# Performance work log

Hardware: AMD Instinct MI355X
Metric: run time of the kernel (lower is better)

## Reference

```python
import jax, jax.numpy as jnp
import numpy as np

N = 50000      # num_labels (nodes)
HID = 64       # hidden_dim
HEADS = 4
CH = 16        # hidden_dim // 4 per head
R = 4          # relations
E = 200000     # edges per relation
DEPTH = 2
SLOPE = 0.2    # GATv2 leaky_relu negative slope
EPS = 1e-5     # LayerNorm eps


def layer_norm(x, g, b):
    mu = jnp.mean(x, axis=-1, keepdims=True)
    var = jnp.mean((x - mu) ** 2, axis=-1, keepdims=True)
    return (x - mu) / jnp.sqrt(var + EPS) * g + b


def setup_inputs() -> dict:
    key = jax.random.key(0)
    ks = jax.random.split(key, 8)
    # edges with src != dst (PyG remove_self_loops is then a no-op)
    src = jax.random.randint(ks[0], (R, E), 0, N, dtype=jnp.int32)
    off = jax.random.randint(ks[1], (R, E), 1, N, dtype=jnp.int32)
    dst = ((src + off) % N).astype(jnp.int32)
    edge_index = jnp.stack([src, dst], axis=1)  # [R, 2, E]
    s = 1.0 / np.sqrt(HID)
    return {
        "label_embeddings": jax.random.normal(ks[2], (N, HID), jnp.float32) * 0.5,
        "entry_w": jax.random.normal(ks[3], (HID, HID), jnp.float32) * s,
        "entry_b": jnp.zeros((HID,), jnp.float32),
        "entry_ln_g": jnp.ones((HID,), jnp.float32),
        "entry_ln_b": jnp.zeros((HID,), jnp.float32),
        "conv_wl": jax.random.normal(ks[4], (DEPTH, R, HID, HEADS * CH), jnp.float32) * s,
        "conv_wr": jax.random.normal(ks[5], (DEPTH, R, HID, HEADS * CH), jnp.float32) * s,
        "conv_att": jax.random.normal(ks[6], (DEPTH, R, HEADS, CH), jnp.float32) * (1.0 / np.sqrt(CH)),
        "conv_bias": jnp.zeros((DEPTH, R, HEADS * CH), jnp.float32),
        "norm_g": jnp.ones((HID,), jnp.float32),
        "norm_b": jnp.zeros((HID,), jnp.float32),
        "edge_index": edge_index,
    }


def _gatv2_layer(x, wl, wr, att, bias, src, dst):
    """One GATv2Conv over one relation. x:[N,HID]; returns [N, HEADS*CH]."""
    xl = (x @ wl).reshape(N, HEADS, CH)  # source transform
    xr = (x @ wr).reshape(N, HEADS, CH)  # target transform
    m = xl[src] + xr[dst]                          # [E+N, HEADS, CH]
    e = jnp.einsum('ehc,hc->eh', jax.nn.leaky_relu(m, SLOPE), att)  # [E+N, HEADS]
    # segment softmax over incoming edges of each dst node
    emax = jax.ops.segment_max(e, dst, num_segments=N)  # [N, HEADS]
    a = jnp.exp(e - emax[dst])
    denom = jax.ops.segment_sum(a, dst, num_segments=N)
    alpha = a / denom[dst]                          # every node has a self-loop -> denom > 0
    msg = xl[src] * alpha[..., None]                # [E+N, HEADS, CH]
    out = jax.ops.segment_sum(msg, dst, num_segments=N).reshape(N, HEADS * CH)
    return out + bias


def reference(label_embeddings, entry_w, entry_b, entry_ln_g, entry_ln_b,
              conv_wl, conv_wr, conv_att, conv_bias, norm_g, norm_b, edge_index):
    x = jax.nn.gelu(layer_norm(label_embeddings @ entry_w + entry_b, entry_ln_g, entry_ln_b),
                    approximate=False)
    loop = jnp.arange(N, dtype=edge_index.dtype)
    for layer in range(DEPTH):
        outs = []
        for r in range(R):
            src = jnp.concatenate([edge_index[r, 0], loop])  # add self-loops (PyG default)
            dst = jnp.concatenate([edge_index[r, 1], loop])
            outs.append(_gatv2_layer(x, conv_wl[layer, r], conv_wr[layer, r],
                                     conv_att[layer, r], conv_bias[layer, r], src, dst))
        x = sum(outs) / R                              # HeteroConv aggr='mean'
        x = layer_norm(jax.nn.gelu(x, approximate=False), norm_g, norm_b)  # dropout = identity (eval)
    return x
```

## Files before the change

kernel.cpp:

```cpp
#include <hip/hip_runtime.h>
#include <hip/hip_bf16.h>

#define NN 50000
#define RR 4
#define EE 200000
#define CAP 32

typedef __hip_bfloat16 bf16;
typedef __attribute__((ext_vector_type(8))) short short8;
typedef __attribute__((ext_vector_type(4))) float float4v;
typedef __attribute__((ext_vector_type(2))) float float2v;

__device__ __forceinline__ float b2f(bf16 v) { return __bfloat162float(v); }
__device__ __forceinline__ unsigned short f2bu(float v) {
    bf16 h = __float2bfloat16(v);
    return *(unsigned short*)&h;
}
__device__ __forceinline__ float ldf(const void* p, int i, int isbf) {
    return isbf ? __bfloat162float(((const bf16*)p)[i]) : ((const float*)p)[i];
}
__device__ __forceinline__ int dtype_isbf(const void* lg) {
    return ((const unsigned*)lg)[0] == 0x3F803F80u;
}
__device__ __forceinline__ float gelu_exact(float x) {
    return 0.5f * x * (1.0f + erff(x * 0.70710678118654752f));
}
__device__ __forceinline__ float2v bp2(unsigned u) {
    float2v f;
    f.x = __uint_as_float(u << 16);
    f.y = __uint_as_float(u & 0xffff0000u);
    return f;
}
__device__ __forceinline__ float2v lrelu2(float2v m) {
    float2v s = m * 0.2f;
    float2v r;
    r.x = fmaxf(m.x, s.x);
    r.y = fmaxf(m.y, s.y);
    return r;
}

#define PW_ENTRY_W 0
#define PW_ENTRY_B 4096
#define PW_LN_G    4160
#define PW_LN_B    4224
#define PW_WL      4288
#define PW_ATT     69824
#define PW_BIAS    70336
#define PW_NG      70848
#define PW_NB      70912
#define PW_TOT     70976

#define WT_ELEMS (2 * RR * 128 * 64)

__global__ __launch_bounds__(1024) void cvt_k(const void* ew, const void* eb, const void* lg,
                                              const void* lb, const void* wl, const void* wr,
                                              const void* at, const void* bi, const void* ng,
                                              const void* nb,
                                              float* __restrict__ P, bf16* __restrict__ WT,
                                              int* __restrict__ cnt) {
    int i = blockIdx.x * 1024 + threadIdx.x;
    int isbf = dtype_isbf(lg);
    if (i < RR * NN) cnt[i] = 0;
    if (i < WT_ELEMS) {
        int k = i & 63;
        int c = (i >> 6) & 127;
        int lr = i >> 13;
        float v = (c < 64) ? ldf(wl, (lr * 64 + k) * 64 + c, isbf)
                           : ldf(wr, (lr * 64 + k) * 64 + (c - 64), isbf);
        WT[i] = __float2bfloat16(v);
    }
    if (i < PW_TOT) {
        const void* src = nullptr;
        int off = 0;
        if (i < PW_ENTRY_B)      { src = ew; off = i - PW_ENTRY_W; }
        else if (i < PW_LN_G)    { src = eb; off = i - PW_ENTRY_B; }
        else if (i < PW_LN_B)    { src = lg; off = i - PW_LN_G; }
        else if (i < PW_WL)      { src = lb; off = i - PW_LN_B; }
        else if (i < PW_ATT)     { src = nullptr; }
        else if (i < PW_BIAS)    { src = at; off = i - PW_ATT; }
        else if (i < PW_NG)      { src = bi; off = i - PW_BIAS; }
        else if (i < PW_NB)      { src = ng; off = i - PW_NG; }
        else                     { src = nb; off = i - PW_NB; }
        if (src) P[i] = ldf(src, off, isbf);
    }
}

#define SCAT_BLOCKS 782
#define ENTRY_BLOCKS 2500
#define ENTRY_WAVES (ENTRY_BLOCKS * 4)
__global__ __launch_bounds__(256) void scent_k(const int* __restrict__ ei,
                                               int* __restrict__ cnt,
                                               unsigned short* __restrict__ col,
                                               const void* __restrict__ emb,
                                               const void* __restrict__ lg,
                                               const float* __restrict__ P,
                                               bf16* __restrict__ xout) {
    int b = blockIdx.x;
    if (b < SCAT_BLOCKS) {
        int base = b * 1024 + threadIdx.x;
#pragma unroll
        for (int j = 0; j < 4; j++) {
            int idx = base + j * 256;
            if (idx < RR * EE) {
                int r = idx / EE;
                int e = idx - r * EE;
                int s = ei[r * 2 * EE + e];
                int d = ei[r * 2 * EE + EE + e];
                int p = atomicAdd(&cnt[r * NN + d], 1);
                if (p < CAP) col[((size_t)r * NN + d) * CAP + p] = (unsigned short)s;
            }
        }
        return;
    }
    int wv = (b - SCAT_BLOCKS) * 4 + (threadIdx.x >> 6);
    int c = threadIdx.x & 63;
    int isbf = dtype_isbf(lg);
    for (int j = 0; j < 5; j++) {
        int node = wv + j * ENTRY_WAVES;
        float ev = ldf(emb, node * 64 + c, isbf);
        float acc = 0.f;
#pragma unroll 8
        for (int k = 0; k < 64; k++) {
            float xv = __shfl(ev, k, 64);
            acc += xv * P[PW_ENTRY_W + k * 64 + c];
        }
        acc += P[PW_ENTRY_B + c];
        float s = acc;
#pragma unroll
        for (int m = 1; m < 64; m <<= 1) s += __shfl_xor(s, m, 64);
        float mu = s * (1.f / 64.f);
        float d = acc - mu;
        float vs = d * d;
#pragma unroll
        for (int m = 1; m < 64; m <<= 1) vs += __shfl_xor(vs, m, 64);
        float var = vs * (1.f / 64.f);
        float y = d * rsqrtf(var + 1e-5f) * P[PW_LN_G + c] + P[PW_LN_B + c];
        xout[node * 64 + c] = __float2bfloat16(gelu_exact(y));
    }
}

#define GR 80
__global__ __launch_bounds__(256) void gemm_m(const bf16* __restrict__ X,
                                              const bf16* __restrict__ WTlayer,
                                              bf16* __restrict__ xlB,
                                              bf16* __restrict__ xrB) {
    int r = blockIdx.y;
    const short* Xs = (const short*)X;
    const short* WT = (const short*)(WTlayer + (size_t)r * 8192);
    bf16* xl = xlB + (size_t)r * NN * 64;
    bf16* xr = xrB + (size_t)r * NN * 64;

    __shared__ float sh[16 * 132];
    int t = threadIdx.x;
    int w = t >> 6;
    int lane = t & 63;
    int m = lane & 15, kq = lane >> 4;
    int row0 = blockIdx.x * GR;

    short8 b0[2], b1[2];
    int c0t[2];
#pragma unroll
    for (int tile = 0; tile < 2; tile++) {
        int ct = w * 2 + tile;
        int c0 = ct * 16 + m;
        c0t[tile] = c0;
        const short* bp = WT + c0 * 64 + kq * 8;
        b0[tile] = *(const short8*)bp;
        b1[tile] = *(const short8*)(bp + 32);
    }

    const short* ap = Xs + (row0 + m) * 64 + kq * 8;
    short8 a0 = *(const short8*)ap;
    short8 a1 = *(const short8*)(ap + 32);

    for (int g = 0; g < 5; g++) {
        short8 na0, na1;
        if (g < 4) {
            const short* np = ap + (g + 1) * 16 * 64;
            na0 = *(const short8*)np;
            na1 = *(const short8*)(np + 32);
        }
#pragma unroll
        for (int tile = 0; tile < 2; tile++) {
            float4v acc = {0.f, 0.f, 0.f, 0.f};
            asm volatile(
                "v_mfma_f32_16x16x32_bf16 %0, %1, %2, %0\n\t"
                "v_mfma_f32_16x16x32_bf16 %0, %3, %4, %0\n\t"
                "s_nop 7\n\t"
                "s_nop 7"
                : "+v"(acc)
                : "v"(a0), "v"(b0[tile]), "v"(a1), "v"(b1[tile]));
#pragma unroll
            for (int i = 0; i < 4; i++) sh[(kq * 4 + i) * 132 + c0t[tile]] = acc[i];
        }
        __syncthreads();
        {
            int row = t >> 4, cg = (t & 15) * 8;
            float v0 = sh[row * 132 + cg + 0], v1 = sh[row * 132 + cg + 1];
            float v2 = sh[row * 132 + cg + 2], v3 = sh[row * 132 + cg + 3];
            float v4 = sh[row * 132 + cg + 4], v5 = sh[row * 132 + cg + 5];
            float v6 = sh[row * 132 + cg + 6], v7 = sh[row * 132 + cg + 7];
            uint4 u;
            u.x = ((unsigned)f2bu(v1) << 16) | f2bu(v0);
            u.y = ((unsigned)f2bu(v3) << 16) | f2bu(v2);
            u.z = ((unsigned)f2bu(v5) << 16) | f2bu(v4);
            u.w = ((unsigned)f2bu(v7) << 16) | f2bu(v6);
            size_t grow = row0 + g * 16 + row;
            if (cg < 64) *(uint4*)&xl[grow * 64 + cg] = u;
            else         *(uint4*)&xr[grow * 64 + (cg - 64)] = u;
        }
        __syncthreads();
        a0 = na0; a1 = na1;
    }
}

__device__ __forceinline__ void edge_accum(uint4 u0, uint4 u1, bool act,
                                           const float2v at2[8], const float2v xr2[8],
                                           float2v A2[8], float& D) {
    float2v x2[8];
    x2[0] = bp2(u0.x); x2[1] = bp2(u0.y); x2[2] = bp2(u0.z); x2[3] = bp2(u0.w);
    x2[4] = bp2(u1.x); x2[5] = bp2(u1.y); x2[6] = bp2(u1.z); x2[7] = bp2(u1.w);
    float2v t2 = (float2v){0.f, 0.f};
#pragma unroll
    for (int i = 0; i < 8; i++)
        t2 = t2 + lrelu2(x2[i] + xr2[i]) * at2[i];
    float tt = t2.x + t2.y;
    float p = act ? exp2f(tt) : 0.f;
    D += p;
    float2v p2 = (float2v){p, p};
#pragma unroll
    for (int i = 0; i < 8; i++) A2[i] = A2[i] + p2 * x2[i];
}

__global__ __launch_bounds__(256) void aggfin_k(const bf16* __restrict__ xlB,
                                                const bf16* __restrict__ xrB,
                                                const float* __restrict__ attL,
                                                const float* __restrict__ biasL,
                                                const int* __restrict__ cnt,
                                                const unsigned short* __restrict__ col,
                                                const float* __restrict__ P,
                                                const void* __restrict__ lg,
                                                void* __restrict__ outp,
                                                int finalOut) {
    __shared__ float shRes[RR][4][68];
    int t = threadIdx.x;
    int r = t >> 6;
    int lane = t & 63;
    int nodeBase = blockIdx.x * 4;
    int nn = lane >> 4, es = (lane >> 2) & 3, h = lane & 3;
    int node = nodeBase + nn;

    const unsigned* xl = (const unsigned*)(xlB + (size_t)r * NN * 64);
    const unsigned* xr = (const unsigned*)(xrB + (size_t)r * NN * 64);
    const float* att = attL + r * 64;
    const float* bias = biasL + r * 64;
    const unsigned short* bucket = col + ((size_t)r * NN + node) * CAP;

    int cn_raw = cnt[r * NN + node];
    int c0raw = (es > 0) ? (int)bucket[es - 1] : node;
    int c1raw = (int)bucket[es + 3];
    const uint4* qr = (const uint4*)(xr + (size_t)node * 32 + h * 8);
    uint4 r0 = qr[0], r1 = qr[1];

    unsigned s0 = (unsigned)c0raw < (unsigned)NN ? (unsigned)c0raw : (unsigned)(NN - 1);
    unsigned s1 = (unsigned)c1raw < (unsigned)NN ? (unsigned)c1raw : (unsigned)(NN - 1);
    const uint4* q0 = (const uint4*)(xl + (size_t)s0 * 32 + h * 8);
    uint4 u0 = q0[0], u1 = q0[1];
    const uint4* q1 = (const uint4*)(xl + (size_t)s1 * 32 + h * 8);
    uint4 w0 = q1[0], w1 = q1[1];

    float2v at2[8], xr2[8];
    {
        const float4* apv = (const float4*)(att + h * 16);
#pragma unroll
        for (int i = 0; i < 4; i++) {
            float4 a = apv[i];
            at2[2 * i].x = a.x * 1.44269504f; at2[2 * i].y = a.y * 1.44269504f;
            at2[2 * i + 1].x = a.z * 1.44269504f; at2[2 * i + 1].y = a.w * 1.44269504f;
        }
        xr2[0] = bp2(r0.x); xr2[1] = bp2(r0.y); xr2[2] = bp2(r0.z); xr2[3] = bp2(r0.w);
        xr2[4] = bp2(r1.x); xr2[5] = bp2(r1.y); xr2[6] = bp2(r1.z); xr2[7] = bp2(r1.w);
    }
    int cn = cn_raw > CAP ? CAP : cn_raw;
    int total = cn + 1;
    int kmax = total;
    kmax = max(kmax, __shfl_xor(kmax, 16, 64));
    kmax = max(kmax, __shfl_xor(kmax, 32, 64));

    float2v A2[8];
#pragma unroll
    for (int i = 0; i < 8; i++) A2[i] = (float2v){0.f, 0.f};
    float D = 0.f;

    edge_accum(u0, u1, es < total, at2, xr2, A2, D);
    edge_accum(w0, w1, es + 4 < total, at2, xr2, A2, D);

    for (int k = es + 8; k < kmax; k += 4) {
        bool act = k < total;
        int sr = act ? (int)bucket[k - 1] : node;
        const uint4* q = (const uint4*)(xl + (size_t)sr * 32 + h * 8);
        uint4 t0 = q[0], t1 = q[1];
        edge_accum(t0, t1, act, at2, xr2, A2, D);
    }

    D += __shfl_xor(D, 4, 64);
    D += __shfl_xor(D, 8, 64);
#pragma unroll
    for (int i = 0; i < 8; i++) {
        A2[i].x += __shfl_xor(A2[i].x, 4, 64);
        A2[i].x += __shfl_xor(A2[i].x, 8, 64);
        A2[i].y += __shfl_xor(A2[i].y, 4, 64);
        A2[i].y += __shfl_xor(A2[i].y, 8, 64);
    }
    if (es == 0) {
        float inv = __builtin_amdgcn_rcpf(D);
        const float4* bp = (const float4*)(bias + h * 16);
        float* dst = &shRes[r][nn][h * 16];
#pragma unroll
        for (int i = 0; i < 4; i++) {
            float4 b = bp[i];
            dst[4 * i + 0] = A2[2 * i].x * inv + b.x;
            dst[4 * i + 1] = A2[2 * i].y * inv + b.y;
            dst[4 * i + 2] = A2[2 * i + 1].x * inv + b.z;
            dst[4 * i + 3] = A2[2 * i + 1].y * inv + b.w;
        }
    }
    __syncthreads();
    int wn = t >> 6, c = t & 63;
    float v = shRes[0][wn][c] + shRes[1][wn][c] + shRes[2][wn][c] + shRes[3][wn][c];
    v = gelu_exact(v * 0.25f);
    float s = v;
#pragma unroll
    for (int m = 1; m < 64; m <<= 1) s += __shfl_xor(s, m, 64);
    float mu = s * (1.f / 64.f);
    float d = v - mu;
    float vs = d * d;
#pragma unroll
    for (int m = 1; m < 64; m <<= 1) vs += __shfl_xor(vs, m, 64);
    float var = vs * (1.f / 64.f);
    float y = d * rsqrtf(var + 1e-5f) * P[PW_NG + c] + P[PW_NB + c];
    size_t o = (size_t)(nodeBase + wn) * 64 + c;
    if (!finalOut) {
        ((bf16*)outp)[o] = __float2bfloat16(y);
    } else {
        if (dtype_isbf(lg)) ((bf16*)outp)[o] = __float2bfloat16(y);
        else                ((float*)outp)[o] = y;
    }
}

extern "C" void kernel_launch(void* const* d_in, const int* in_sizes, int n_in,
                              void* d_out, int out_size, void* d_ws, size_t ws_size,
                              hipStream_t stream) {
    const void* emb = d_in[0];
    const void* lg  = d_in[3];
    const int*  ei  = (const int*)d_in[11];

    const size_t BUF = (size_t)NN * 64;

    bf16* X   = (bf16*)d_ws;
    bf16* XL  = X + BUF;
    bf16* XR  = XL + RR * BUF;
    bf16* WT  = XR + RR * BUF;
    float* P  = (float*)(WT + WT_ELEMS);
    int* cnt  = (int*)(P + PW_TOT);
    unsigned short* col = (unsigned short*)(cnt + RR * NN);

    int cvtN = RR * NN;
    cvt_k<<<(cvtN + 1023) / 1024, 1024, 0, stream>>>(d_in[1], d_in[2], d_in[3], d_in[4],
                                                     d_in[5], d_in[6], d_in[7], d_in[8],
                                                     d_in[9], d_in[10], P, WT, cnt);

    scent_k<<<SCAT_BLOCKS + ENTRY_BLOCKS, 256, 0, stream>>>(ei, cnt, col, emb, lg, P, X);

    int gemmBlocks = NN / GR;
    int nodeBlocks = NN / 4;

    for (int l = 0; l < 2; l++) {
        gemm_m<<<dim3(gemmBlocks, RR), 256, 0, stream>>>(X, WT + (size_t)l * RR * 8192, XL, XR);
        aggfin_k<<<nodeBlocks, 256, 0, stream>>>(
            XL, XR, P + PW_ATT + (size_t)l * RR * 64, P + PW_BIAS + (size_t)l * RR * 64,
            cnt, col, P, lg, (l == 0) ? (void*)X : d_out, l);
    }
}
```

Before: 334.8 us.

## Replace fixed-capacity adjacency buckets with CSR built via histogram, scan, scatter

Replaces the per-node CAP=32 bucket array with a compact CSR layout. A histogram pass records each edge's slot, a three-kernel prefix scan produces row pointers, and the scatter runs inside the first-layer GEMM launch as extra blocks. This shrinks the adjacency footprint and removes the capacity truncation, which improves gather locality in the aggregation kernel. The cost is three extra small launches and an extra read of the edge list.

Result: faster. 323.6 us (-3.3%).

```diff
diff --git a/kernel.cpp b/kernel.cpp
--- a/kernel.cpp
+++ b/kernel.cpp
@@ -4,14 +4,12 @@
 #define NN 50000
 #define RR 4
 #define EE 200000
-#define CAP 32
 
 typedef __hip_bfloat16 bf16;
 typedef __attribute__((ext_vector_type(8))) short short8;
 typedef __attribute__((ext_vector_type(4))) float float4v;
 typedef __attribute__((ext_vector_type(2))) float float2v;
 
-__device__ __forceinline__ float b2f(bf16 v) { return __bfloat162float(v); }
 __device__ __forceinline__ unsigned short f2bu(float v) {
     bf16 h = __float2bfloat16(v);
     return *(unsigned short*)&h;
@@ -51,6 +49,9 @@
 #define PW_TOT     70976
 
 #define WT_ELEMS (2 * RR * 128 * 64)
+#define SCAN_N (RR * NN)
+#define NSB 196
+#define ESB 196
 
 __global__ __launch_bounds__(1024) void cvt_k(const void* ew, const void* eb, const void* lg,
                                               const void* lb, const void* wl, const void* wr,
@@ -60,7 +61,7 @@
                                               int* __restrict__ cnt) {
     int i = blockIdx.x * 1024 + threadIdx.x;
     int isbf = dtype_isbf(lg);
-    if (i < RR * NN) cnt[i] = 0;
+    if (i < SCAN_N) cnt[i] = 0;
     if (i < WT_ELEMS) {
         int k = i & 63;
         int c = (i >> 6) & 127;
@@ -85,18 +86,18 @@
     }
 }
 
-#define SCAT_BLOCKS 782
+#define HIST_BLOCKS 782
 #define ENTRY_BLOCKS 2500
 #define ENTRY_WAVES (ENTRY_BLOCKS * 4)
 __global__ __launch_bounds__(256) void scent_k(const int* __restrict__ ei,
                                                int* __restrict__ cnt,
-                                               unsigned short* __restrict__ col,
+                                               unsigned char* __restrict__ slot8,
                                                const void* __restrict__ emb,
                                                const void* __restrict__ lg,
                                                const float* __restrict__ P,
                                                bf16* __restrict__ xout) {
     int b = blockIdx.x;
-    if (b < SCAT_BLOCKS) {
+    if (b < HIST_BLOCKS) {
         int base = b * 1024 + threadIdx.x;
 #pragma unroll
         for (int j = 0; j < 4; j++) {
@@ -104,15 +105,14 @@
             if (idx < RR * EE) {
                 int r = idx / EE;
                 int e = idx - r * EE;
-                int s = ei[r * 2 * EE + e];
                 int d = ei[r * 2 * EE + EE + e];
                 int p = atomicAdd(&cnt[r * NN + d], 1);
-                if (p < CAP) col[((size_t)r * NN + d) * CAP + p] = (unsigned short)s;
+                slot8[idx] = (unsigned char)p;
             }
         }
         return;
     }
-    int wv = (b - SCAT_BLOCKS) * 4 + (threadIdx.x >> 6);
+    int wv = (b - HIST_BLOCKS) * 4 + (threadIdx.x >> 6);
     int c = threadIdx.x & 63;
     int isbf = dtype_isbf(lg);
     for (int j = 0; j < 5; j++) {
@@ -139,12 +139,100 @@
     }
 }
 
+__global__ __launch_bounds__(256) void scanA_k(const int* __restrict__ cnt,
+                                               int* __restrict__ bsum) {
+    int b = blockIdx.x, t = threadIdx.x;
+    int s = 0;
+#pragma unroll
+    for (int j = 0; j < 4; j++) {
+        int i = b * 1024 + j * 256 + t;
+        if (i < SCAN_N) s += cnt[i];
+    }
+#pragma unroll
+    for (int m = 1; m < 64; m <<= 1) s += __shfl_xor(s, m, 64);
+    __shared__ int ws[4];
+    if ((t & 63) == 0) ws[t >> 6] = s;
+    __syncthreads();
+    if (t == 0) bsum[b] = ws[0] + ws[1] + ws[2] + ws[3];
+}
+
+__global__ void scanB_k(int* __restrict__ bsum, int* __restrict__ rp) {
+    int l = threadIdx.x;
+    int i0 = l * 4;
+    int v0 = (i0 + 0 < NSB) ? bsum[i0 + 0] : 0;
+    int v1 = (i0 + 1 < NSB) ? bsum[i0 + 1] : 0;
+    int v2 = (i0 + 2 < NSB) ? bsum[i0 + 2] : 0;
+    int v3 = (i0 + 3 < NSB) ? bsum[i0 + 3] : 0;
+    int ts = v0 + v1 + v2 + v3;
+    int inc = ts;
+#pragma unroll
+    for (int m = 1; m < 64; m <<= 1) {
+        int y = __shfl_up(inc, m, 64);
+        if (l >= m) inc += y;
+    }
+    int run = inc - ts;
+    if (i0 + 0 < NSB) { bsum[i0 + 0] = run; run += v0; }
+    if (i0 + 1 < NSB) { bsum[i0 + 1] = run; run += v1; }
+    if (i0 + 2 < NSB) { bsum[i0 + 2] = run; run += v2; }
+    if (i0 + 3 < NSB) { bsum[i0 + 3] = run; run += v3; }
+    if (l == 63) rp[SCAN_N] = inc;
+}
+
+__global__ __launch_bounds__(256) void scanC_k(const int* __restrict__ cnt,
+                                               const int* __restrict__ bsum,
+                                               int* __restrict__ rp) {
+    int b = blockIdx.x, t = threadIdx.x;
+    int i0 = b * 1024 + t * 4;
+    int v0 = (i0 + 0 < SCAN_N) ? cnt[i0 + 0] : 0;
+    int v1 = (i0 + 1 < SCAN_N) ? cnt[i0 + 1] : 0;
+    int v2 = (i0 + 2 < SCAN_N) ? cnt[i0 + 2] : 0;
+    int v3 = (i0 + 3 < SCAN_N) ? cnt[i0 + 3] : 0;
+    int ts = v0 + v1 + v2 + v3;
+    int lane = t & 63, w = t >> 6;
+    int inc = ts;
+#pragma unroll
+    for (int m = 1; m < 64; m <<= 1) {
+        int y = __shfl_up(inc, m, 64);
+        if (lane >= m) inc += y;
+    }
+    __shared__ int ws[4];
+    if (lane == 63) ws[w] = inc;
+    __syncthreads();
+    int run = bsum[b];
+    for (int k = 0; k < w; k++) run += ws[k];
+    run += inc - ts;
+    if (i0 + 0 < SCAN_N) { rp[i0 + 0] = run; run += v0; }
+    if (i0 + 1 < SCAN_N) { rp[i0 + 1] = run; run += v1; }
+    if (i0 + 2 < SCAN_N) { rp[i0 + 2] = run; run += v2; }
+    if (i0 + 3 < SCAN_N) { rp[i0 + 3] = run; run += v3; }
+}
+
 #define GR 80
 __global__ __launch_bounds__(256) void gemm_m(const bf16* __restrict__ X,
                                               const bf16* __restrict__ WTlayer,
                                               bf16* __restrict__ xlB,
-                                              bf16* __restrict__ xrB) {
+                                              bf16* __restrict__ xrB,
+                                              const int* __restrict__ ei,
+                                              const unsigned char* __restrict__ slot8,
+                                              const int* __restrict__ rp,
+                                              unsigned short* __restrict__ col,
+                                              int scatBlocks) {
+    int bx = blockIdx.x;
     int r = blockIdx.y;
+    if (bx < scatBlocks) {
+        const int* eis = ei + r * 2 * EE;
+#pragma unroll
+        for (int j = 0; j < 4; j++) {
+            int e = bx * 1024 + j * 256 + threadIdx.x;
+            if (e < EE) {
+                int s = eis[e];
+                int d = eis[EE + e];
+                int p = slot8[r * EE + e];
+                col[rp[r * NN + d] + p] = (unsigned short)s;
+            }
+        }
+        return;
+    }
     const short* Xs = (const short*)X;
     const short* WT = (const short*)(WTlayer + (size_t)r * 8192);
     bf16* xl = xlB + (size_t)r * NN * 64;
@@ -155,7 +243,7 @@
     int w = t >> 6;
     int lane = t & 63;
     int m = lane & 15, kq = lane >> 4;
-    int row0 = blockIdx.x * GR;
+    int row0 = (bx - scatBlocks) * GR;
 
     short8 b0[2], b1[2];
     int c0t[2];
@@ -236,7 +324,7 @@
                                                 const bf16* __restrict__ xrB,
                                                 const float* __restrict__ attL,
                                                 const float* __restrict__ biasL,
-                                                const int* __restrict__ cnt,
+                                                const int* __restrict__ rp,
                                                 const unsigned short* __restrict__ col,
                                                 const float* __restrict__ P,
                                                 const void* __restrict__ lg,
@@ -254,13 +342,16 @@
     const unsigned* xr = (const unsigned*)(xrB + (size_t)r * NN * 64);
     const float* att = attL + r * 64;
     const float* bias = biasL + r * 64;
-    const unsigned short* bucket = col + ((size_t)r * NN + node) * CAP;
-
-    int cn_raw = cnt[r * NN + node];
+
+    int idx = r * NN + node;
+    int base = rp[idx];
+    int cn = rp[idx + 1] - base;
+    const uint4* qr = (const uint4*)(xr + (size_t)node * 32 + h * 8);
+    uint4 r0 = qr[0], r1 = qr[1];
+
+    const unsigned short* bucket = col + base;
     int c0raw = (es > 0) ? (int)bucket[es - 1] : node;
     int c1raw = (int)bucket[es + 3];
-    const uint4* qr = (const uint4*)(xr + (size_t)node * 32 + h * 8);
-    uint4 r0 = qr[0], r1 = qr[1];
 
     unsigned s0 = (unsigned)c0raw < (unsigned)NN ? (unsigned)c0raw : (unsigned)(NN - 1);
     unsigned s1 = (unsigned)c1raw < (unsigned)NN ? (unsigned)c1raw : (unsigned)(NN - 1);
@@ -281,7 +372,6 @@
         xr2[0] = bp2(r0.x); xr2[1] = bp2(r0.y); xr2[2] = bp2(r0.z); xr2[3] = bp2(r0.w);
         xr2[4] = bp2(r1.x); xr2[5] = bp2(r1.y); xr2[6] = bp2(r1.z); xr2[7] = bp2(r1.w);
     }
-    int cn = cn_raw > CAP ? CAP : cn_raw;
     int total = cn + 1;
     int kmax = total;
     kmax = max(kmax, __shfl_xor(kmax, 16, 64));
@@ -363,22 +453,31 @@
     bf16* WT  = XR + RR * BUF;
     float* P  = (float*)(WT + WT_ELEMS);
     int* cnt  = (int*)(P + PW_TOT);
-    unsigned short* col = (unsigned short*)(cnt + RR * NN);
-
-    int cvtN = RR * NN;
+    int* rp   = cnt + SCAN_N;
+    int* bsum = rp + SCAN_N + 1;
+    unsigned short* col = (unsigned short*)(bsum + 256);
+    unsigned char* slot8 = (unsigned char*)(col + RR * EE + 64);
+
+    int cvtN = SCAN_N;
     cvt_k<<<(cvtN + 1023) / 1024, 1024, 0, stream>>>(d_in[1], d_in[2], d_in[3], d_in[4],
                                                      d_in[5], d_in[6], d_in[7], d_in[8],
                                                      d_in[9], d_in[10], P, WT, cnt);
 
-    scent_k<<<SCAT_BLOCKS + ENTRY_BLOCKS, 256, 0, stream>>>(ei, cnt, col, emb, lg, P, X);
-
-    int gemmBlocks = NN / GR;
+    scent_k<<<HIST_BLOCKS + ENTRY_BLOCKS, 256, 0, stream>>>(ei, cnt, slot8, emb, lg, P, X);
+
+    scanA_k<<<NSB, 256, 0, stream>>>(cnt, bsum);
+    scanB_k<<<1, 64, 0, stream>>>(bsum, rp);
+    scanC_k<<<NSB, 256, 0, stream>>>(cnt, bsum, rp);
+
+    int gemmBlocks = 625;
     int nodeBlocks = NN / 4;
 
     for (int l = 0; l < 2; l++) {
-        gemm_m<<<dim3(gemmBlocks, RR), 256, 0, stream>>>(X, WT + (size_t)l * RR * 8192, XL, XR);
+        int sb = (l == 0) ? ESB : 0;
+        gemm_m<<<dim3(sb + gemmBlocks, RR), 256, 0, stream>>>(
+            X, WT + (size_t)l * RR * 8192, XL, XR, ei, slot8, rp, col, sb);
         aggfin_k<<<nodeBlocks, 256, 0, stream>>>(
             XL, XR, P + PW_ATT + (size_t)l * RR * 64, P + PW_BIAS + (size_t)l * RR * 64,
-            cnt, col, P, lg, (l == 0) ? (void*)X : d_out, l);
-    }
-}
+            rp, col, P, lg, (l == 0) ? (void*)X : d_out, l);
+    }
+}
```
